# Kernel tuning notes

Hardware: AMD Instinct MI355X
Metric: run time of the kernel (lower is better)

The kernel has to match this reference:

```python
import jax, jax.numpy as jnp
import numpy as np
import math

B, T, D, H = 2, 2048, 1024, 16
DH = D // H          # 64
NB = DH // 2         # 32 rope blocks
EPS = 1e-5


def _layernorm(x, g, b):
    m = jnp.mean(x, axis=-1, keepdims=True)
    v = jnp.var(x, axis=-1, keepdims=True)
    return (x - m) * jax.lax.rsqrt(v + EPS) * g + b


def _rope(x, cos, sin):
    # x: (B,H,T,DH); cos/sin: (B,H,T,NB)
    x1 = x[..., 0::2]
    x2 = x[..., 1::2]
    o1 = x1 * cos - x2 * sin
    o2 = x1 * sin + x2 * cos
    return jnp.stack([o1, o2], axis=-1).reshape(x.shape)


def setup_inputs() -> dict:
    key = jax.random.key(0)
    ks = jax.random.split(key, 16)
    x = jax.random.normal(ks[0], (B, T, D), dtype=jnp.float32)
    # genuine RoPE angles broadcast to (B,H,T,NB)
    inv_freq = 1.0 / (10000.0 ** (np.arange(NB, dtype=np.float32) / NB))
    ang = jnp.asarray(np.arange(T, dtype=np.float32)[:, None] * inv_freq[None, :])  # (T,NB)
    cos_a = jnp.broadcast_to(jnp.cos(ang)[None, None], (B, H, T, NB)).astype(jnp.float32)
    sin_a = jnp.broadcast_to(jnp.sin(ang)[None, None], (B, H, T, NB)).astype(jnp.float32)
    causal_mask = jnp.triu(jnp.ones((T, T), dtype=bool), k=1)  # True above diagonal -> masked
    s = 0.02
    def w(k, shp):
        return jax.random.normal(k, shp, dtype=jnp.float32) * s
    return {
        "x": x, "cos_a": cos_a, "sin_a": sin_a, "causal_mask": causal_mask,
        "Wq": w(ks[1], (D, D)), "bq": jnp.zeros((D,), jnp.float32),
        "Wk": w(ks[2], (D, D)), "bk": jnp.zeros((D,), jnp.float32),
        "Wv": w(ks[3], (D, D)), "bv": jnp.zeros((D,), jnp.float32),
        "Wo": w(ks[4], (D, D)), "bo": jnp.zeros((D,), jnp.float32),
        "g1": jnp.ones((D,), jnp.float32), "b1n": jnp.zeros((D,), jnp.float32),
        "g2": jnp.ones((D,), jnp.float32), "b2n": jnp.zeros((D,), jnp.float32),
        "W1": w(ks[5], (D, 4 * D)), "bf1": jnp.zeros((4 * D,), jnp.float32),
        "W2": w(ks[6], (4 * D, D)), "bf2": jnp.zeros((D,), jnp.float32),
    }


def reference(x, cos_a, sin_a, causal_mask, Wq, bq, Wk, bk, Wv, bv, Wo, bo,
              g1, b1n, g2, b2n, W1, bf1, W2, bf2):
    h = _layernorm(x, g1, b1n)
    def heads(y):
        return y.reshape(B, T, H, DH).transpose(0, 2, 1, 3)  # (B,H,T,DH)
    Q = heads(h @ Wq + bq)
    K = heads(h @ Wk + bk)
    V = heads(h @ Wv + bv)
    Q = _rope(Q, cos_a, sin_a)
    K = _rope(K, cos_a, sin_a)
    scale = math.sqrt(DH)
    scores = jnp.einsum('bhqd,bhkd->bhqk', Q, K) / scale
    scores = jnp.where(causal_mask[None, None], -jnp.inf, scores)
    attn = jax.nn.softmax(scores, axis=-1)
    out = jnp.einsum('bhqk,bhkd->bhqd', attn, V)
    out = out.transpose(0, 2, 1, 3).reshape(B, T, D)
    out = out @ Wo + bo
    x = x + out  # dropout=0.0 (eval)
    h2 = _layernorm(x, g2, b2n)
    ffn = jax.nn.gelu(h2 @ W1 + bf1, approximate=False) @ W2 + bf2
    return x + ffn
```

## Files before the change

### kernel.cpp

```cpp
#include <hip/hip_runtime.h>

typedef unsigned short u16;
typedef unsigned int   u32;
typedef __attribute__((ext_vector_type(8))) short          short8;
typedef __attribute__((ext_vector_type(4))) float          f32x4;
typedef __attribute__((ext_vector_type(8))) unsigned short u16x8;
typedef __attribute__((ext_vector_type(4))) unsigned short u16x4;

#define T_SEQ  2048
#define DMODEL 1024
#define NHEAD  16
#define DHEAD  64
#define HBUF   4194304

__device__ __forceinline__ float bf2f(u16 u) {
    u32 i = ((u32)u) << 16; float f; __builtin_memcpy(&f, &i, 4); return f;
}
__device__ __forceinline__ u16 f2bf(float f) {
    u32 x; __builtin_memcpy(&x, &f, 4);
    return (u16)((x + 0x7FFFu + ((x >> 16) & 1u)) >> 16);
}

__device__ __forceinline__ void gld16(const u16* g, u16* l) {
    auto gp = reinterpret_cast<const __attribute__((address_space(1))) u32*>(
        reinterpret_cast<uintptr_t>(g));
    auto lp = reinterpret_cast<__attribute__((address_space(3))) u32*>(
        (u32)reinterpret_cast<uintptr_t>(l));
    __builtin_amdgcn_global_load_lds(gp, lp, 16, 0, 0);
}

template<int N> __device__ __forceinline__ void wait_vmcnt() {
    if constexpr (N == 0)      asm volatile("s_waitcnt vmcnt(0)" ::: "memory");
    else if constexpr (N == 2) asm volatile("s_waitcnt vmcnt(2)" ::: "memory");
    else if constexpr (N == 3) asm volatile("s_waitcnt vmcnt(3)" ::: "memory");
    else                       asm volatile("s_waitcnt vmcnt(4)" ::: "memory");
}

__device__ __forceinline__ void xcd_swz(int& bx, int& by) {
    int gx = gridDim.x;
    int nwg = gx * gridDim.y;
    int w = by * gx + bx;
    int L = (w & 7) * (nwg >> 3) + (w >> 3);
    bx = L % gx; by = L / gx;
}

__global__ __launch_bounds__(256) void ln_k(const float* __restrict__ x,
                                            const float* __restrict__ g,
                                            const float* __restrict__ bb,
                                            u16* __restrict__ out)
{
    int row = blockIdx.x, tid = threadIdx.x;
    const float* xr = x + (size_t)row * DMODEL;
    f32x4 v = *(const f32x4*)(xr + tid * 4);
    float s  = v[0] + v[1] + v[2] + v[3];
    float s2 = v[0]*v[0] + v[1]*v[1] + v[2]*v[2] + v[3]*v[3];
    #pragma unroll
    for (int o = 32; o; o >>= 1) { s += __shfl_xor(s, o); s2 += __shfl_xor(s2, o); }
    __shared__ float rs[4], rq[4];
    if ((tid & 63) == 0) { rs[tid >> 6] = s; rq[tid >> 6] = s2; }
    __syncthreads();
    float S  = rs[0] + rs[1] + rs[2] + rs[3];
    float S2 = rq[0] + rq[1] + rq[2] + rq[3];
    float mean = S * (1.f / DMODEL);
    float var  = S2 * (1.f / DMODEL) - mean * mean;
    float rstd = rsqrtf(var + 1e-5f);
    f32x4 gv = *(const f32x4*)(g + tid * 4);
    f32x4 bv = *(const f32x4*)(bb + tid * 4);
    u16x4 o;
    #pragma unroll
    for (int e = 0; e < 4; e++)
        o[e] = f2bf((v[e] - mean) * rstd * gv[e] + bv[e]);
    *(u16x4*)(out + (size_t)row * DMODEL + tid * 4) = o;
}

__device__ __forceinline__ void tr_body(const float* __restrict__ in,
                                        u16* __restrict__ out, int R, int C,
                                        int bx, int by, int tid)
{
    __shared__ u16 s[64][72];
    int c0 = bx * 64, r0 = by * 64;
    #pragma unroll
    for (int p = 0; p < 2; p++) {
        int r = (tid >> 3) + p * 32, cq = (tid & 7) * 8;
        const float* ip = in + (size_t)(r0 + r) * C + c0 + cq;
        f32x4 a = *(const f32x4*)ip;
        f32x4 b = *(const f32x4*)(ip + 4);
        u16x8 o;
        #pragma unroll
        for (int e = 0; e < 4; e++) { o[e] = f2bf(a[e]); o[4 + e] = f2bf(b[e]); }
        *(u16x8*)(&s[r][cq]) = o;
    }
    __syncthreads();
    int oc = tid >> 2, kq = (tid & 3) * 16;
    u16 tmp[16] __attribute__((aligned(16)));
    #pragma unroll
    for (int e = 0; e < 16; e++) tmp[e] = s[kq + e][oc];
    u16* op = out + (size_t)(c0 + oc) * R + r0 + kq;
    *(u16x8*)op       = *(const u16x8*)(&tmp[0]);
    *(u16x8*)(op + 8) = *(const u16x8*)(&tmp[8]);
}

__global__ __launch_bounds__(256) void trall_k(const float* __restrict__ w0, const float* __restrict__ w1,
                                               const float* __restrict__ w2, const float* __restrict__ w3,
                                               const float* __restrict__ wf1, const float* __restrict__ wf2,
                                               u16* __restrict__ o0, u16* __restrict__ o1,
                                               u16* __restrict__ o2, u16* __restrict__ o3,
                                               u16* __restrict__ of1, u16* __restrict__ of2)
{
    int z = blockIdx.z;
    if (z < 4) {
        const float* in = (z == 0) ? w0 : (z == 1) ? w1 : (z == 2) ? w2 : w3;
        u16* out        = (z == 0) ? o0 : (z == 1) ? o1 : (z == 2) ? o2 : o3;
        tr_body(in, out, 1024, 1024, blockIdx.x, blockIdx.y, threadIdx.x);
    } else if (z < 8) {
        tr_body(wf1, of1, 1024, 4096, blockIdx.x + 16 * (z - 4), blockIdx.y, threadIdx.x);
    } else {
        tr_body(wf2, of2, 4096, 1024, blockIdx.x, blockIdx.y + 16 * (z - 8), threadIdx.x);
    }
}

constexpr int EPI_QKV = 0, EPI_RESF = 1, EPI_GELU = 2, EPI_RES2 = 3;

template<int EPI>
__device__ __forceinline__ void epi_elem(
    float v, int m, int n, int N, void* outv,
    const float* b0, const float* resid)
{
    if constexpr (EPI == EPI_RESF) {
        v += b0[n] + resid[(size_t)m * N + n];
        ((float*)outv)[(size_t)m * N + n] = v;
    } else if constexpr (EPI == EPI_GELU) {
        v += b0[n];
        float gl = 0.5f * v * (1.f + erff(v * 0.70710678118654752f));
        ((u16*)outv)[(size_t)m * N + n] = f2bf(gl);
    } else {
        v += b0[n] + resid[(size_t)m * N + n];
        ((float*)outv)[(size_t)m * N + n] = v;
    }
}

template<int EPI>
__global__ __launch_bounds__(512) void gemm8_k(
    const u16* __restrict__ A, const u16* __restrict__ Bt, void* __restrict__ outv,
    int M, int N, int K, int Kld,
    const float* __restrict__ b0, const float* __restrict__ b1, const float* __restrict__ b2,
    const float* __restrict__ resid,
    const float* __restrict__ cosp, const float* __restrict__ sinp)
{
    (void)M;
    constexpr int TSZ = 128 * 32;
    __shared__ u16 As[3 * TSZ];
    __shared__ u16 Bs[3 * TSZ];
    int tid = threadIdx.x;
    int bx = blockIdx.x, by = blockIdx.y;
    xcd_swz(bx, by);
    int n0 = bx * 128, m0 = by * 128;
    int wave = tid >> 6, lane = tid & 63, lm = lane & 15, ko = lane >> 4;
    int wm2 = wave >> 2, wn2 = wave & 3;

    f32x4 acc[4][2];
    #pragma unroll
    for (int i = 0; i < 4; i++)
        #pragma unroll
        for (int j = 0; j < 2; j++) acc[i][j] = (f32x4){0.f, 0.f, 0.f, 0.f};

    int srow = tid >> 2;
    int scol = (tid & 3) * 8;
    const u16* Ag = A  + (size_t)(m0 + srow) * Kld + scol;
    const u16* Bg = Bt + (size_t)(n0 + srow) * Kld + scol;
    u16* Al = &As[wave * 16 * 32];
    u16* Bl = &Bs[wave * 16 * 32];

    auto issue = [&](int t, int b) {
        gld16(Ag + t * 32, Al + b * TSZ);
        gld16(Bg + t * 32, Bl + b * TSZ);
    };

    int NT = K >> 5;
    issue(0, 0);
    issue(1, 1);

    int bc = 0, bn = 2;
    for (int kt = 0; kt < NT; kt++) {
        if (kt + 1 < NT) wait_vmcnt<2>();
        else             wait_vmcnt<0>();
        __builtin_amdgcn_s_barrier();
        __builtin_amdgcn_sched_barrier(0);
        if (kt + 2 < NT) issue(kt + 2, bn);

        const u16* Ab = &As[bc * TSZ];
        const u16* Bb = &Bs[bc * TSZ];
        short8 af[4], bf[2];
        #pragma unroll
        for (int i = 0; i < 4; i++)
            af[i] = *(const short8*)(&Ab[(wm2 * 64 + i * 16 + lm) * 32 + ko * 8]);
        #pragma unroll
        for (int j = 0; j < 2; j++)
            bf[j] = *(const short8*)(&Bb[(wn2 * 32 + j * 16 + lm) * 32 + ko * 8]);
        __builtin_amdgcn_s_setprio(1);
        #pragma unroll
        for (int i = 0; i < 4; i++)
            #pragma unroll
            for (int j = 0; j < 2; j++)
                acc[i][j] = __builtin_amdgcn_mfma_f32_16x16x32_bf16(af[i], bf[j], acc[i][j], 0, 0, 0);
        __builtin_amdgcn_s_setprio(0);
        bc = (bc == 2) ? 0 : bc + 1;
        bn = (bn == 2) ? 0 : bn + 1;
    }

    #pragma unroll
    for (int i = 0; i < 4; i++) {
        #pragma unroll
        for (int j = 0; j < 2; j++) {
            int n = n0 + wn2 * 32 + j * 16 + lm;
            int mb = m0 + wm2 * 64 + i * 16 + ko * 4;
            if constexpr (EPI == EPI_QKV) {
                int which = n >> 10, nn = n & 1023;
                const float* bp = (which == 0) ? b0 : (which == 1 ? b1 : b2);
                float bias = bp[nn];
                int bi = mb >> 11, t2b = mb & 2047;
                int hh = nn >> 6, d = nn & 63;
                u16* outp = (u16*)outv + (size_t)which * HBUF;
                if (which == 2) {
                    u16x4 o;
                    #pragma unroll
                    for (int r = 0; r < 4; r++) o[r] = f2bf(acc[i][j][r] + bias);
                    *(u16x4*)(&outp[((size_t)((bi * NHEAD + hh) * DHEAD + d)) * T_SEQ + t2b]) = o;
                } else {
                    #pragma unroll
                    for (int r = 0; r < 4; r++) {
                        float v = acc[i][j][r] + bias;
                        float vp = __shfl_xor(v, 1);
                        int t2 = t2b + r;
                        size_t ci = (size_t)t2 * 32 + (d >> 1);
                        float c = cosp[ci], sn2 = sinp[ci];
                        float o = (d & 1) ? (vp * sn2 + v * c) : (v * c - vp * sn2);
                        if (which == 0) o *= 0.18033688f;
                        outp[((size_t)((bi * NHEAD + hh) * T_SEQ + t2)) * DHEAD + d] = f2bf(o);
                    }
                }
            } else {
                #pragma unroll
                for (int r = 0; r < 4; r++)
                    epi_elem<EPI>(acc[i][j][r], mb + r, n, N, outv, b0, resid);
            }
        }
    }
}

__device__ __forceinline__ void attn_step(
    bool diag, int wave, int lm, int ko,
    short8 aq0, short8 aq1,
    const u16 (*sK)[72], const u16 (*sV)[72], u16 (*sPw)[72],
    f32x4* oacc, float* lr)
{
    f32x4 sacc[4];
    #pragma unroll
    for (int j = 0; j < 4; j++) {
        short8 bk0 = *(const short8*)(&sK[j * 16 + lm][ko * 8]);
        short8 bk1 = *(const short8*)(&sK[j * 16 + lm][32 + ko * 8]);
        f32x4 z = (f32x4){0.f, 0.f, 0.f, 0.f};
        z = __builtin_amdgcn_mfma_f32_16x16x32_bf16(aq0, bk0, z, 0, 0, 0);
        z = __builtin_amdgcn_mfma_f32_16x16x32_bf16(aq1, bk1, z, 0, 0, 0);
        sacc[j] = z;
    }
    if (diag) {
        #pragma unroll
        for (int j = 0; j < 4; j++)
            #pragma unroll
            for (int r = 0; r < 4; r++)
                if (j * 16 + lm > wave * 16 + ko * 4 + r) sacc[j][r] = -1e30f;
    }

    u16 pb[4][4];
    #pragma unroll
    for (int j = 0; j < 4; j++)
        #pragma unroll
        for (int r = 0; r < 4; r++) {
            float p = __builtin_amdgcn_exp2f(sacc[j][r]);
            lr[r] += p;
            pb[j][r] = f2bf(p);
        }

    #pragma unroll
    for (int j = 0; j < 4; j++)
        #pragma unroll
        for (int r = 0; r < 4; r++) sPw[ko * 4 + r][j * 16 + lm] = pb[j][r];

    #pragma unroll
    for (int ks = 0; ks < 2; ks++) {
        short8 ap = *(const short8*)(&sPw[lm][ks * 32 + ko * 8]);
        #pragma unroll
        for (int j = 0; j < 4; j++) {
            short8 bv = *(const short8*)(&sV[j * 16 + lm][ks * 32 + ko * 8]);
            oacc[j] = __builtin_amdgcn_mfma_f32_16x16x32_bf16(ap, bv, oacc[j], 0, 0, 0);
        }
    }
}

__global__ __launch_bounds__(256) void fattn_k(const u16* __restrict__ Q,
                                               const u16* __restrict__ K,
                                               const u16* __restrict__ Vt,
                                               u16* __restrict__ out)
{
    __shared__ u16 sQP[4][16][72];
    __shared__ u16 sK[2][64][72];
    __shared__ u16 sV[2][64][72];
    int tid = threadIdx.x;
    int qtA = blockIdx.x;
    int qtB = 31 - qtA;
    int bh = blockIdx.y;
    int wave = tid >> 6, lane = tid & 63, lm = lane & 15, ko = lane >> 4;
    int bi = bh >> 4, hh = bh & 15;

    const u16* Kb = K  + (size_t)bh * T_SEQ * DHEAD;
    const u16* Vb = Vt + (size_t)bh * DHEAD * T_SEQ;
    u16* sQf = &sQP[0][0][0];
    int srow = tid >> 2, scol = (tid & 3) * 16;

    short8 aqA0, aqA1, aqB0, aqB1;
    {
        const u16* QbA = Q + ((size_t)bh * T_SEQ + qtA * 64) * DHEAD + (size_t)srow * DHEAD + scol;
        *(u16x8*)(&sQf[srow * 72 + scol])     = *(const u16x8*)QbA;
        *(u16x8*)(&sQf[srow * 72 + scol + 8]) = *(const u16x8*)(QbA + 8);
        __syncthreads();
        aqA0 = *(const short8*)(&sQf[(wave * 16 + lm) * 72 + ko * 8]);
        aqA1 = *(const short8*)(&sQf[(wave * 16 + lm) * 72 + 32 + ko * 8]);
        __syncthreads();
        const u16* QbB = Q + ((size_t)bh * T_SEQ + qtB * 64) * DHEAD + (size_t)srow * DHEAD + scol;
        *(u16x8*)(&sQf[srow * 72 + scol])     = *(const u16x8*)QbB;
        *(u16x8*)(&sQf[srow * 72 + scol + 8]) = *(const u16x8*)(QbB + 8);
        __syncthreads();
        aqB0 = *(const short8*)(&sQf[(wave * 16 + lm) * 72 + ko * 8]);
        aqB1 = *(const short8*)(&sQf[(wave * 16 + lm) * 72 + 32 + ko * 8]);
    }

    f32x4 oA[4], oB[4];
    float lA[4], lB[4];
    #pragma unroll
    for (int j = 0; j < 4; j++) { oA[j] = (f32x4){0,0,0,0}; oB[j] = (f32x4){0,0,0,0}; }
    #pragma unroll
    for (int r = 0; r < 4; r++) { lA[r] = 0.f; lB[r] = 0.f; }

    int nA = qtA + 1, n = nA + qtB + 1;

    u16x8 pk0, pk1, pv0, pv1;
    {
        const u16* kp = Kb + (size_t)srow * DHEAD + scol;
        pk0 = *(const u16x8*)kp; pk1 = *(const u16x8*)(kp + 8);
        const u16* vp = Vb + (size_t)srow * T_SEQ + scol;
        pv0 = *(const u16x8*)vp; pv1 = *(const u16x8*)(vp + 8);
    }

    for (int i = 0; i < n; i++) {
        bool isA = i < nA;
        int kt = isA ? i : i - nA;
        int buf = i & 1;

        *(u16x8*)(&sK[buf][srow][scol])     = pk0;
        *(u16x8*)(&sK[buf][srow][scol + 8]) = pk1;
        *(u16x8*)(&sV[buf][srow][scol])     = pv0;
        *(u16x8*)(&sV[buf][srow][scol + 8]) = pv1;

        if (i + 1 < n) {
            int kt2 = (i + 1 < nA) ? i + 1 : i + 1 - nA;
            const u16* kp = Kb + ((size_t)(kt2 * 64 + srow)) * DHEAD + scol;
            pk0 = *(const u16x8*)kp; pk1 = *(const u16x8*)(kp + 8);
            const u16* vp = Vb + (size_t)srow * T_SEQ + kt2 * 64 + scol;
            pv0 = *(const u16x8*)vp; pv1 = *(const u16x8*)(vp + 8);
        }

        __syncthreads();

        if (isA)
            attn_step(kt == qtA, wave, lm, ko, aqA0, aqA1, sK[buf], sV[buf], sQP[wave], oA, lA);
        else
            attn_step(kt == qtB, wave, lm, ko, aqB0, aqB1, sK[buf], sV[buf], sQP[wave], oB, lB);
    }

    #pragma unroll
    for (int o = 1; o < 16; o <<= 1)
        #pragma unroll
        for (int r = 0; r < 4; r++) { lA[r] += __shfl_xor(lA[r], o); lB[r] += __shfl_xor(lB[r], o); }
    #pragma unroll
    for (int r = 0; r < 4; r++) { lA[r] = 1.f / lA[r]; lB[r] = 1.f / lB[r]; }
    int qrowA = qtA * 64 + wave * 16, qrowB = qtB * 64 + wave * 16;
    #pragma unroll
    for (int j = 0; j < 4; j++)
        #pragma unroll
        for (int r = 0; r < 4; r++) {
            out[((size_t)(bi * T_SEQ) + qrowA + ko * 4 + r) * DMODEL + hh * DHEAD + j * 16 + lm]
                = f2bf(oA[j][r] * lA[r]);
            out[((size_t)(bi * T_SEQ) + qrowB + ko * 4 + r) * DMODEL + hh * DHEAD + j * 16 + lm]
                = f2bf(oB[j][r] * lB[r]);
        }
}

extern "C" void kernel_launch(void* const* d_in, const int* in_sizes, int n_in,
                              void* d_out, int out_size, void* d_ws, size_t ws_size,
                              hipStream_t stream)
{
    (void)in_sizes; (void)n_in; (void)out_size; (void)ws_size;
    const float* x    = (const float*)d_in[0];
    const float* cosp = (const float*)d_in[1];
    const float* sinp = (const float*)d_in[2];
    const float* Wq  = (const float*)d_in[4];
    const float* bq  = (const float*)d_in[5];
    const float* Wk  = (const float*)d_in[6];
    const float* bk  = (const float*)d_in[7];
    const float* Wv  = (const float*)d_in[8];
    const float* bv  = (const float*)d_in[9];
    const float* Wo  = (const float*)d_in[10];
    const float* bo  = (const float*)d_in[11];
    const float* g1  = (const float*)d_in[12];
    const float* b1n = (const float*)d_in[13];
    const float* g2  = (const float*)d_in[14];
    const float* b2n = (const float*)d_in[15];
    const float* W1  = (const float*)d_in[16];
    const float* bf1 = (const float*)d_in[17];
    const float* W2  = (const float*)d_in[18];
    const float* bf2 = (const float*)d_in[19];

    char* ws = (char*)d_ws;
    const size_t MB = 1024 * 1024;
    u16*   qkvT  = (u16*)(ws + 0);
    u16*   WoT   = (u16*)(ws + 6 * MB);
    u16*   W1T   = (u16*)(ws + 8 * MB);
    u16*   W2T   = (u16*)(ws + 16 * MB);
    u16*   h     = (u16*)(ws + 24 * MB);
    u16*   qkvh  = (u16*)(ws + 32 * MB);
    u16*   attnC = (u16*)(ws + 56 * MB);
    float* x2    = (float*)(ws + 64 * MB);
    u16*   ffnh  = (u16*)(ws + 80 * MB);

    trall_k<<<dim3(16, 16, 12), 256, 0, stream>>>(
        Wq, Wk, Wv, Wo, W1, W2,
        qkvT, qkvT + 1 * MB, qkvT + 2 * MB, WoT, W1T, W2T);

    ln_k<<<4096, 256, 0, stream>>>(x, g1, b1n, h);
    gemm8_k<EPI_QKV><<<dim3(24, 32), 512, 0, stream>>>(
        h, qkvT, qkvh, 4096, 3072, 1024, 1024, bq, bk, bv, nullptr, cosp, sinp);
    fattn_k<<<dim3(16, 32), 256, 0, stream>>>(qkvh, qkvh + HBUF, qkvh + 2 * HBUF, attnC);
    gemm8_k<EPI_RESF><<<dim3(8, 32), 512, 0, stream>>>(
        attnC, WoT, x2, 4096, 1024, 1024, 1024, bo, nullptr, nullptr, x, nullptr, nullptr);
    ln_k<<<4096, 256, 0, stream>>>(x2, g2, b2n, h);
    gemm8_k<EPI_GELU><<<dim3(32, 32), 512, 0, stream>>>(
        h, W1T, ffnh, 4096, 4096, 1024, 1024, bf1, nullptr, nullptr, nullptr, nullptr, nullptr);
    gemm8_k<EPI_RES2><<<dim3(8, 32), 512, 0, stream>>>(
        ffnh, W2T, (float*)d_out, 4096, 1024, 4096, 4096, bf2, nullptr, nullptr, x2, nullptr, nullptr);
}
```

Measured before the change: 375.1 us.

## Add 128x64 GEMM tile for N=1024 GEMMs and XOR-swizzle LDS tiles

Templates the GEMM on the N tile width. The two N=1024 GEMMs (output projection and FFN down-projection) now use 128x64 tiles, which doubles their grid from 256 to 512 blocks so more of the CUs are busy. Only half the threads load B in that path, so the vmcnt waits are split per wave. It also XOR-swizzles the k-chunk column in shared memory for both the stores and the fragment reads, to reduce LDS bank conflicts. The cost is less operand reuse per block with 64-wide tiles and more complex wait logic.

```diff
diff --git a/kernel.cpp b/kernel.cpp
--- a/kernel.cpp
+++ b/kernel.cpp
@@ -31,8 +31,8 @@
 
 template<int N> __device__ __forceinline__ void wait_vmcnt() {
     if constexpr (N == 0)      asm volatile("s_waitcnt vmcnt(0)" ::: "memory");
+    else if constexpr (N == 1) asm volatile("s_waitcnt vmcnt(1)" ::: "memory");
     else if constexpr (N == 2) asm volatile("s_waitcnt vmcnt(2)" ::: "memory");
-    else if constexpr (N == 3) asm volatile("s_waitcnt vmcnt(3)" ::: "memory");
     else                       asm volatile("s_waitcnt vmcnt(4)" ::: "memory");
 }
 
@@ -139,7 +139,7 @@
     }
 }
 
-template<int EPI>
+template<int EPI, int BN>
 __global__ __launch_bounds__(512) void gemm8_k(
     const u16* __restrict__ A, const u16* __restrict__ Bt, void* __restrict__ outv,
     int M, int N, int K, int Kld,
@@ -148,58 +148,69 @@
     const float* __restrict__ cosp, const float* __restrict__ sinp)
 {
     (void)M;
-    constexpr int TSZ = 128 * 32;
-    __shared__ u16 As[3 * TSZ];
-    __shared__ u16 Bs[3 * TSZ];
+    constexpr int ASZ = 128 * 32;
+    constexpr int BSZ = BN * 32;
+    constexpr int MI  = (BN == 128) ? 4 : 2;
+    constexpr int MR  = MI * 16;
+    __shared__ u16 As[3 * ASZ];
+    __shared__ u16 Bs[3 * BSZ];
     int tid = threadIdx.x;
     int bx = blockIdx.x, by = blockIdx.y;
     xcd_swz(bx, by);
-    int n0 = bx * 128, m0 = by * 128;
+    int n0 = bx * BN, m0 = by * 128;
     int wave = tid >> 6, lane = tid & 63, lm = lane & 15, ko = lane >> 4;
-    int wm2 = wave >> 2, wn2 = wave & 3;
-
-    f32x4 acc[4][2];
-    #pragma unroll
-    for (int i = 0; i < 4; i++)
+    int wn_i = (BN == 128) ? (wave & 3) : (wave & 1);
+    int wm_i = (BN == 128) ? (wave >> 2) : (wave >> 1);
+
+    f32x4 acc[MI][2];
+    #pragma unroll
+    for (int i = 0; i < MI; i++)
         #pragma unroll
         for (int j = 0; j < 2; j++) acc[i][j] = (f32x4){0.f, 0.f, 0.f, 0.f};
 
     int srow = tid >> 2;
-    int scol = (tid & 3) * 8;
+    int scol = (((tid & 3) ^ (srow & 3))) * 8;
     const u16* Ag = A  + (size_t)(m0 + srow) * Kld + scol;
     const u16* Bg = Bt + (size_t)(n0 + srow) * Kld + scol;
     u16* Al = &As[wave * 16 * 32];
     u16* Bl = &Bs[wave * 16 * 32];
 
     auto issue = [&](int t, int b) {
-        gld16(Ag + t * 32, Al + b * TSZ);
-        gld16(Bg + t * 32, Bl + b * TSZ);
+        gld16(Ag + t * 32, Al + b * ASZ);
+        if constexpr (BN == 128) {
+            gld16(Bg + t * 32, Bl + b * BSZ);
+        } else {
+            if (tid < 256) gld16(Bg + t * 32, Bl + b * BSZ);
+        }
     };
 
     int NT = K >> 5;
     issue(0, 0);
     issue(1, 1);
 
+    int kos = (ko ^ (lm & 3)) * 8;
     int bc = 0, bn = 2;
     for (int kt = 0; kt < NT; kt++) {
-        if (kt + 1 < NT) wait_vmcnt<2>();
-        else             wait_vmcnt<0>();
+        if (kt + 1 < NT) {
+            if constexpr (BN == 128) wait_vmcnt<2>();
+            else { if (wave < 4) wait_vmcnt<2>(); else wait_vmcnt<1>(); }
+        } else wait_vmcnt<0>();
         __builtin_amdgcn_s_barrier();
         __builtin_amdgcn_sched_barrier(0);
         if (kt + 2 < NT) issue(kt + 2, bn);
 
-        const u16* Ab = &As[bc * TSZ];
-        const u16* Bb = &Bs[bc * TSZ];
-        short8 af[4], bf[2];
-        #pragma unroll
-        for (int i = 0; i < 4; i++)
-            af[i] = *(const short8*)(&Ab[(wm2 * 64 + i * 16 + lm) * 32 + ko * 8]);
+        const u16* Ab = &As[bc * ASZ];
+        const u16* Bb = &Bs[bc * BSZ];
+        short8 af[MI], bf[2];
+        #pragma unroll
+        for (int i = 0; i < MI; i++)
+            af[i] = *(const short8*)(&Ab[(wm_i * MR + i * 16 + lm) * 32 + kos]);
         #pragma unroll
         for (int j = 0; j < 2; j++)
-            bf[j] = *(const short8*)(&Bb[(wn2 * 32 + j * 16 + lm) * 32 + ko * 8]);
+            bf[j] = *(const short8*)(&Bb[(wn_i * 32 + j * 16 + lm) * 32 + kos]);
         __builtin_amdgcn_s_setprio(1);
         #pragma unroll
-        for (int i = 0; i < 4; i++)
+        for (int i = 0; i < MI; i++)
             #pragma unroll
             for (int j = 0; j < 2; j++)
                 acc[i][j] = __builtin_amdgcn_mfma_f32_16x16x32_bf16(af[i], bf[j], acc[i][j], 0, 0, 0);
@@ -209,11 +220,11 @@
     }
 
     #pragma unroll
-    for (int i = 0; i < 4; i++) {
+    for (int i = 0; i < MI; i++) {
         #pragma unroll
         for (int j = 0; j < 2; j++) {
-            int n = n0 + wn2 * 32 + j * 16 + lm;
-            int mb = m0 + wm2 * 64 + i * 16 + ko * 4;
+            int n = n0 + wn_i * 32 + j * 16 + lm;
+            int mb = m0 + wm_i * MR + i * 16 + ko * 4;
             if constexpr (EPI == EPI_QKV) {
                 int which = n >> 10, nn = n & 1023;
                 const float* bp = (which == 0) ? b0 : (which == 1 ? b1 : b2);
@@ -438,14 +449,14 @@
         qkvT, qkvT + 1 * MB, qkvT + 2 * MB, WoT, W1T, W2T);
 
     ln_k<<<4096, 256, 0, stream>>>(x, g1, b1n, h);
-    gemm8_k<EPI_QKV><<<dim3(24, 32), 512, 0, stream>>>(
+    gemm8_k<EPI_QKV, 128><<<dim3(24, 32), 512, 0, stream>>>(
         h, qkvT, qkvh, 4096, 3072, 1024, 1024, bq, bk, bv, nullptr, cosp, sinp);
     fattn_k<<<dim3(16, 32), 256, 0, stream>>>(qkvh, qkvh + HBUF, qkvh + 2 * HBUF, attnC);
-    gemm8_k<EPI_RESF><<<dim3(8, 32), 512, 0, stream>>>(
+    gemm8_k<EPI_RESF, 64><<<dim3(16, 32), 512, 0, stream>>>(
         attnC, WoT, x2, 4096, 1024, 1024, 1024, bo, nullptr, nullptr, x, nullptr, nullptr);
     ln_k<<<4096, 256, 0, stream>>>(x2, g2, b2n, h);
-    gemm8_k<EPI_GELU><<<dim3(32, 32), 512, 0, stream>>>(
+    gemm8_k<EPI_GELU, 128><<<dim3(32, 32), 512, 0, stream>>>(
         h, W1T, ffnh, 4096, 4096, 1024, 1024, bf1, nullptr, nullptr, nullptr, nullptr, nullptr);
-    gemm8_k<EPI_RES2><<<dim3(8, 32), 512, 0, stream>>>(
+    gemm8_k<EPI_RES2, 64><<<dim3(16, 32), 512, 0, stream>>>(
         ffnh, W2T, (float*)d_out, 4096, 1024, 4096, 4096, bf2, nullptr, nullptr, x2, nullptr, nullptr);
 }
```

Result: no change. 381.2 us (+1.6%).

## Template GEMM on N-tile width, use 256-wide tiles for QKV and FFN1

Applied to the files above, without the earlier changes.

Makes the bf16 GEMM's N tile a template parameter and launches the QKV and FFN-up GEMMs with 128x256 tiles, so each A tile is reused across twice as many columns. The LDS staging layout changes to a contiguous 16-row-per-wave arrangement. Fragments are read with explicit ds_read_b128 inline asm followed by a full lgkmcnt wait. launch_bounds also gains a min-blocks hint. The cost is more accumulator registers and LDS per block, and fewer blocks in the grid, which may lower occupancy and worsen tail behaviour.

```diff
diff --git a/kernel.cpp b/kernel.cpp
--- a/kernel.cpp
+++ b/kernel.cpp
@@ -6,6 +6,7 @@
 typedef __attribute__((ext_vector_type(4))) float          f32x4;
 typedef __attribute__((ext_vector_type(8))) unsigned short u16x8;
 typedef __attribute__((ext_vector_type(4))) unsigned short u16x4;
+typedef __attribute__((ext_vector_type(4))) u32            u32x4;
 
 #define T_SEQ  2048
 #define DMODEL 1024
@@ -28,6 +29,13 @@
         (u32)reinterpret_cast<uintptr_t>(l));
     __builtin_amdgcn_global_load_lds(gp, lp, 16, 0, 0);
 }
+
+__device__ __forceinline__ short8 dsr128(u32 addr) {
+    u32x4 r;
+    asm volatile("ds_read_b128 %0, %1" : "=&v"(r) : "v"(addr));
+    return __builtin_bit_cast(short8, r);
+}
+#define LGKM0() { asm volatile("s_waitcnt lgkmcnt(0)" ::: "memory"); __builtin_amdgcn_sched_barrier(0); }
 
 template<int N> __device__ __forceinline__ void wait_vmcnt() {
     if constexpr (N == 0)      asm volatile("s_waitcnt vmcnt(0)" ::: "memory");
@@ -139,8 +147,8 @@
     }
 }
 
-template<int EPI>
-__global__ __launch_bounds__(512) void gemm8_k(
+template<int EPI, int BN>
+__global__ __launch_bounds__(512, 4) void gemm8_k(
     const u16* __restrict__ A, const u16* __restrict__ Bt, void* __restrict__ outv,
     int M, int N, int K, int Kld,
     const float* __restrict__ b0, const float* __restrict__ b1, const float* __restrict__ b2,
@@ -148,60 +156,69 @@
     const float* __restrict__ cosp, const float* __restrict__ sinp)
 {
     (void)M;
-    constexpr int TSZ = 128 * 32;
-    __shared__ u16 As[3 * TSZ];
-    __shared__ u16 Bs[3 * TSZ];
+    constexpr int ASZ = 128 * 32;
+    constexpr int BSZ = BN * 32;
+    constexpr int NJ  = BN / 64;
+    constexpr int LPT = 1 + BN / 128;
+    __shared__ u16 As[3 * ASZ];
+    __shared__ u16 Bs[3 * BSZ];
     int tid = threadIdx.x;
     int bx = blockIdx.x, by = blockIdx.y;
     xcd_swz(bx, by);
-    int n0 = bx * 128, m0 = by * 128;
+    int n0 = bx * BN, m0 = by * 128;
     int wave = tid >> 6, lane = tid & 63, lm = lane & 15, ko = lane >> 4;
-    int wm2 = wave >> 2, wn2 = wave & 3;
-
-    f32x4 acc[4][2];
+    int wm = wave >> 2, wn = wave & 3;
+
+    f32x4 acc[4][NJ];
     #pragma unroll
     for (int i = 0; i < 4; i++)
         #pragma unroll
-        for (int j = 0; j < 2; j++) acc[i][j] = (f32x4){0.f, 0.f, 0.f, 0.f};
-
-    int srow = tid >> 2;
-    int scol = (tid & 3) * 8;
-    const u16* Ag = A  + (size_t)(m0 + srow) * Kld + scol;
-    const u16* Bg = Bt + (size_t)(n0 + srow) * Kld + scol;
-    u16* Al = &As[wave * 16 * 32];
-    u16* Bl = &Bs[wave * 16 * 32];
+        for (int j = 0; j < NJ; j++) acc[i][j] = (f32x4){0.f, 0.f, 0.f, 0.f};
+
+    int sr = lane & 15, sg = lane >> 4;
+    const u16* Ag  = A  + (size_t)(m0 + wave * 16 + sr) * Kld + sg * 8;
+    const u16* Bg  = Bt + (size_t)(n0 + wave * 16 + sr) * Kld + sg * 8;
+    const u16* Bg2 = Bt + (size_t)(n0 + 128 + wave * 16 + sr) * Kld + sg * 8;
+    u16* Al = &As[wave * 512];
+    u16* Bl = &Bs[wave * 512];
 
     auto issue = [&](int t, int b) {
-        gld16(Ag + t * 32, Al + b * TSZ);
-        gld16(Bg + t * 32, Bl + b * TSZ);
+        gld16(Ag + t * 32, Al + b * ASZ);
+        gld16(Bg + t * 32, Bl + b * BSZ);
+        if constexpr (BN == 256) gld16(Bg2 + t * 32, Bl + b * BSZ + 4096);
     };
 
     int NT = K >> 5;
     issue(0, 0);
     issue(1, 1);
 
+    const u32 Asb = (u32)(uintptr_t)&As[0];
+    const u32 Bsb = (u32)(uintptr_t)&Bs[0];
+    const u32 lb  = (u32)(lane * 16);
+
     int bc = 0, bn = 2;
     for (int kt = 0; kt < NT; kt++) {
-        if (kt + 1 < NT) wait_vmcnt<2>();
+        if (kt + 1 < NT) wait_vmcnt<LPT>();
         else             wait_vmcnt<0>();
         __builtin_amdgcn_s_barrier();
         __builtin_amdgcn_sched_barrier(0);
         if (kt + 2 < NT) issue(kt + 2, bn);
 
-        const u16* Ab = &As[bc * TSZ];
-        const u16* Bb = &Bs[bc * TSZ];
-        short8 af[4], bf[2];
+        u32 Ab = Asb + (u32)(bc * (ASZ * 2));
+        u32 Bb = Bsb + (u32)(bc * (BSZ * 2));
+        short8 af[4], bf[NJ];
         #pragma unroll
         for (int i = 0; i < 4; i++)
-            af[i] = *(const short8*)(&Ab[(wm2 * 64 + i * 16 + lm) * 32 + ko * 8]);
-        #pragma unroll
-        for (int j = 0; j < 2; j++)
-            bf[j] = *(const short8*)(&Bb[(wn2 * 32 + j * 16 + lm) * 32 + ko * 8]);
+            af[i] = dsr128(Ab + (u32)((wm * 4 + i) * 1024) + lb);
+        #pragma unroll
+        for (int j = 0; j < NJ; j++)
+            bf[j] = dsr128(Bb + (u32)((wn * NJ + j) * 1024) + lb);
+        LGKM0();
         __builtin_amdgcn_s_setprio(1);
         #pragma unroll
         for (int i = 0; i < 4; i++)
             #pragma unroll
-            for (int j = 0; j < 2; j++)
+            for (int j = 0; j < NJ; j++)
                 acc[i][j] = __builtin_amdgcn_mfma_f32_16x16x32_bf16(af[i], bf[j], acc[i][j], 0, 0, 0);
         __builtin_amdgcn_s_setprio(0);
         bc = (bc == 2) ? 0 : bc + 1;
@@ -211,9 +228,9 @@
     #pragma unroll
     for (int i = 0; i < 4; i++) {
         #pragma unroll
-        for (int j = 0; j < 2; j++) {
-            int n = n0 + wn2 * 32 + j * 16 + lm;
-            int mb = m0 + wm2 * 64 + i * 16 + ko * 4;
+        for (int j = 0; j < NJ; j++) {
+            int n = n0 + wn * (NJ * 16) + j * 16 + lm;
+            int mb = m0 + wm * 64 + i * 16 + ko * 4;
             if constexpr (EPI == EPI_QKV) {
                 int which = n >> 10, nn = n & 1023;
                 const float* bp = (which == 0) ? b0 : (which == 1 ? b1 : b2);
@@ -438,14 +455,14 @@
         qkvT, qkvT + 1 * MB, qkvT + 2 * MB, WoT, W1T, W2T);
 
     ln_k<<<4096, 256, 0, stream>>>(x, g1, b1n, h);
-    gemm8_k<EPI_QKV><<<dim3(24, 32), 512, 0, stream>>>(
+    gemm8_k<EPI_QKV, 256><<<dim3(12, 32), 512, 0, stream>>>(
         h, qkvT, qkvh, 4096, 3072, 1024, 1024, bq, bk, bv, nullptr, cosp, sinp);
     fattn_k<<<dim3(16, 32), 256, 0, stream>>>(qkvh, qkvh + HBUF, qkvh + 2 * HBUF, attnC);
-    gemm8_k<EPI_RESF><<<dim3(8, 32), 512, 0, stream>>>(
+    gemm8_k<EPI_RESF, 128><<<dim3(8, 32), 512, 0, stream>>>(
         attnC, WoT, x2, 4096, 1024, 1024, 1024, bo, nullptr, nullptr, x, nullptr, nullptr);
     ln_k<<<4096, 256, 0, stream>>>(x2, g2, b2n, h);
-    gemm8_k<EPI_GELU><<<dim3(32, 32), 512, 0, stream>>>(
+    gemm8_k<EPI_GELU, 256><<<dim3(16, 32), 512, 0, stream>>>(
         h, W1T, ffnh, 4096, 4096, 1024, 1024, bf1, nullptr, nullptr, nullptr, nullptr, nullptr);
-    gemm8_k<EPI_RES2><<<dim3(8, 32), 512, 0, stream>>>(
+    gemm8_k<EPI_RES2, 128><<<dim3(8, 32), 512, 0, stream>>>(
         ffnh, W2T, (float*)d_out, 4096, 1024, 4096, 4096, bf2, nullptr, nullptr, x2, nullptr, nullptr);
 }
```

New measurement: 412.4 us. 1.1x slower.
